# Optimization experiments

Hardware: AMD Instinct MI355X
Metric: run time of the kernel (lower is better)

The kernel has to match this reference:

```python
import jax, jax.numpy as jnp
import numpy as np
from itertools import product

N_VOX = 100000
GRID = 128
KS = 3
K = KS ** 3
INC_MAX, OUTC_MAX = 64, 96
RUNTIME_INC, RUNTIME_OUTC = 48, 64


def _build_rulebook(rng):
    flat = rng.choice(GRID ** 3, size=N_VOX, replace=False).astype(np.int64)
    coords = np.stack(np.unravel_index(flat, (GRID, GRID, GRID)), axis=1)  # [N,3]
    # Dense lookup table: flat coord -> voxel index (or -1).
    table = np.full(GRID ** 3, -1, dtype=np.int32)
    table[flat] = np.arange(N_VOX, dtype=np.int32)
    offsets = np.array(list(product([-1, 0, 1], repeat=3)), dtype=np.int64)  # [27,3]
    idx = np.empty((K, N_VOX), dtype=np.int32)
    for k, off in enumerate(offsets):
        nb = coords + off  # stride=1, dilation=1
        valid = np.all((nb >= 0) & (nb < GRID), axis=1)
        nb_flat = (nb[:, 0] * GRID + nb[:, 1]) * GRID + nb[:, 2]
        nb_flat = np.where(valid, nb_flat, 0)
        idx[k] = np.where(valid, table[nb_flat], -1)
    return idx


def setup_inputs() -> dict:
    key = jax.random.key(0)
    kf, kw = jax.random.split(key)
    features = jax.random.normal(kf, (N_VOX, RUNTIME_INC), dtype=jnp.float32)
    # Full kernel param [K, inc_max, outc_max]; runtime-sliced inside reference.
    std = 1.0 / np.sqrt(INC_MAX * K)
    kernel = jax.random.uniform(kw, (K, INC_MAX, OUTC_MAX), dtype=jnp.float32,
                                minval=-std, maxval=std)
    idx = jnp.asarray(_build_rulebook(np.random.default_rng(0)))  # [K, N]
    return {"features": features, "kernel": kernel, "idx": idx,
            "runtime_inc": RUNTIME_INC, "runtime_outc": RUNTIME_OUTC}


def reference(features, kernel, idx, runtime_inc, runtime_outc):
    # Dynamic channel slicing (static Python ints -> jit friendly).
    w = kernel[:, :runtime_inc, :runtime_outc]          # [K, Ci, Co]
    mask = idx >= 0                                      # [K, N]
    safe = jnp.where(mask, idx, 0)
    # Gather -> per-offset GEMM -> accumulate (scatter is identity: out idx == n).
    gathered = features[safe] * mask[..., None].astype(features.dtype)  # [K, N, Ci]
    out = jnp.einsum('knc,kco->no', gathered, w)         # [N, Co]
    return out
```

## Files before the change

### kernel.cpp

```cpp
#include <hip/hip_runtime.h>
#include <hip/hip_bf16.h>


#define NVOX       100000
#define INC        48
#define INC_MAX    64
#define OUTC       64
#define OUTC_MAX   96
#define KOFF       27
#define FEAT_ROW   64
#define FEATB_ELEMS ((NVOX + 1) * FEAT_ROW)
#define WTB_ELEMS  (KOFF * 4096)
#define WS_NEED    ((size_t)(FEATB_ELEMS + WTB_ELEMS) * 2)
#define FEAT_THREADS ((NVOX + 1) * 8)
#define FEAT_PREP_BLKS ((FEAT_THREADS + 255) / 256)
#define WTB_PREP_BLKS  432
#define MAIN_BLOCKS 782

typedef __attribute__((ext_vector_type(8))) short  short8;
typedef __attribute__((ext_vector_type(4))) float  floatx4;

__device__ __forceinline__ short f2bf(float f) {
    union { __hip_bfloat16 h; short s; } u;
    u.h = __float2bfloat16(f);
    return u.s;
}

__global__ void __launch_bounds__(256)
prep_cvt(const float* __restrict__ feat, const float* __restrict__ wk,
         short* __restrict__ featb, short* __restrict__ wtb)
{
    int b = blockIdx.x;
    if (b < FEAT_PREP_BLKS) {
        int t = b * 256 + threadIdx.x;
        if (t < FEAT_THREADS) {
            int g = t >> 3, c8 = (t & 7) * 8;
            short8 p = (short8){0, 0, 0, 0, 0, 0, 0, 0};
            if (g < NVOX && c8 < INC) {
                const floatx4* src = (const floatx4*)(feat + g * INC + c8);
                floatx4 f0 = src[0], f1 = src[1];
                #pragma unroll
                for (int j = 0; j < 4; ++j) { p[j] = f2bf(f0[j]); p[4 + j] = f2bf(f1[j]); }
            }
            *(short8*)(featb + g * FEAT_ROW + c8) = p;
        }
    } else {
        int t = (b - FEAT_PREP_BLKS) * 256 + threadIdx.x;
        int k = t >> 12, r = t & 4095;
        int frag = r >> 9, lane = (r >> 3) & 63, j = t & 7;
        int ks = frag >> 2, nt = frag & 3, quad = lane >> 4, l16 = lane & 15;
        int o = nt * 16 + l16, c = ks * 32 + quad * 8 + j;
        wtb[t] = (c < INC) ? f2bf(wk[k * (INC_MAX * OUTC_MAX) + c * OUTC_MAX + o])
                           : (short)0;
    }
}

__global__ void __launch_bounds__(256, 3)
spconv_main(const short* __restrict__ featb, const short* __restrict__ wtb,
            const int* __restrict__ idx, float* __restrict__ out)
{
    __shared__ short Bs[2][2][4096];

    const int tid  = threadIdx.x;
    const int lane = tid & 63;
    const int wave = tid >> 6;
    const int quad = lane >> 4;
    const int l16  = lane & 15;

    int bid = blockIdx.x;
    int sb  = (bid < 776) ? ((bid & 7) * 97 + (bid >> 3)) : bid;

    const int m0 = (sb * 4 + wave) * 32;
    const int r0 = m0 + l16;
    const int r1 = m0 + 16 + l16;
    const bool v0 = r0 < NVOX, v1 = r1 < NVOX;
    const int rr0 = v0 ? r0 : 0;
    const int rr1 = v1 ? r1 : 0;

    floatx4 acc[2][4];
    #pragma unroll
    for (int i = 0; i < 2; ++i)
        #pragma unroll
        for (int j = 0; j < 4; ++j)
            acc[i][j] = (floatx4){0.f, 0.f, 0.f, 0.f};

    short8 A[4][2][2];
    short8 bst[4][2];
    int    row0[4], row1[4];

    auto ldrow = [&](int k) {
        int t0 = idx[k * NVOX + rr0];
        int t1 = idx[k * NVOX + rr1];
        row0[k & 3] = (t0 < 0) ? NVOX : t0;
        row1[k & 3] = (t1 < 0) ? NVOX : t1;
    };
    auto aload = [&](int k) {
        const short8* p0 = (const short8*)(featb + row0[k & 3] * FEAT_ROW);
        const short8* p1 = (const short8*)(featb + row1[k & 3] * FEAT_ROW);
        A[k & 3][0][0] = p0[quad];  A[k & 3][0][1] = p0[quad + 4];
        A[k & 3][1][0] = p1[quad];  A[k & 3][1][1] = p1[quad + 4];
    };
    auto bload = [&](int k) {
        bst[k & 3][0] = *(const short8*)(wtb + k * 4096 + tid * 8);
        bst[k & 3][1] = *(const short8*)(wtb + k * 4096 + tid * 8 + 2048);
    };
    auto compute = [&](int k, int pb, int sub) {
        #pragma unroll
        for (int ks = 0; ks < 2; ++ks) {
            short8 b[4];
            #pragma unroll
            for (int nt = 0; nt < 4; ++nt)
                b[nt] = *(const short8*)&Bs[pb][sub][(ks * 4 + nt) * 512 + lane * 8];
            #pragma unroll
            for (int mt = 0; mt < 2; ++mt)
                #pragma unroll
                for (int nt = 0; nt < 4; ++nt)
                    acc[mt][nt] = __builtin_amdgcn_mfma_f32_16x16x32_bf16(
                        A[k & 3][mt][ks], b[nt], acc[mt][nt], 0, 0, 0);
        }
    };

    ldrow(0); ldrow(1); ldrow(2); ldrow(3);
    aload(0); aload(1);
    bload(0); bload(1);

    #pragma unroll
    for (int j = 0; j < 14; ++j) {
        const int kk = 2 * j;
        const int pb = j & 1;

        *(short8*)&Bs[pb][0][tid * 8]        = bst[kk & 3][0];
        *(short8*)&Bs[pb][0][tid * 8 + 2048] = bst[kk & 3][1];
        if (kk + 1 < KOFF) {
            *(short8*)&Bs[pb][1][tid * 8]        = bst[(kk + 1) & 3][0];
            *(short8*)&Bs[pb][1][tid * 8 + 2048] = bst[(kk + 1) & 3][1];
        }
        __syncthreads();

        if (kk + 2 < KOFF) { aload(kk + 2); bload(kk + 2); }
        if (kk + 3 < KOFF) { aload(kk + 3); bload(kk + 3); }
        if (kk + 4 < KOFF) ldrow(kk + 4);
        if (kk + 5 < KOFF) ldrow(kk + 5);

        compute(kk, pb, 0);
        if (kk + 1 < KOFF) compute(kk + 1, pb, 1);
    }

    #pragma unroll
    for (int mt = 0; mt < 2; ++mt) {
        int gbase = m0 + mt * 16 + quad * 4;
        #pragma unroll
        for (int r = 0; r < 4; ++r) {
            if (gbase + r < NVOX) {
                #pragma unroll
                for (int nt = 0; nt < 4; ++nt)
                    out[(gbase + r) * OUTC + nt * 16 + l16] = acc[mt][nt][r];
            }
        }
    }
}

__global__ void __launch_bounds__(256)
spconv_fallback(const float* __restrict__ feat, const float* __restrict__ wk,
                const int* __restrict__ idx, float* __restrict__ out)
{
    int t = blockIdx.x * 256 + threadIdx.x;
    if (t >= NVOX * OUTC) return;
    int n = t >> 6, o = t & 63;
    float s = 0.f;
    for (int k = 0; k < KOFF; ++k) {
        int g = idx[k * NVOX + n];
        if (g >= 0) {
            const float* fr = feat + g * INC;
            const float* wr = wk + k * (INC_MAX * OUTC_MAX) + o;
            #pragma unroll 8
            for (int c = 0; c < INC; ++c) s += fr[c] * wr[c * OUTC_MAX];
        }
    }
    out[t] = s;
}

extern "C" void kernel_launch(void* const* d_in, const int* in_sizes, int n_in,
                              void* d_out, int out_size, void* d_ws, size_t ws_size,
                              hipStream_t stream) {
    const float* feat = (const float*)d_in[0];
    const float* wk   = (const float*)d_in[1];
    const int*   idx  = (const int*)d_in[2];
    float* out = (float*)d_out;

    if (ws_size >= WS_NEED) {
        short* featb = (short*)d_ws;
        short* wtb   = featb + FEATB_ELEMS;
        prep_cvt<<<FEAT_PREP_BLKS + WTB_PREP_BLKS, 256, 0, stream>>>(feat, wk, featb, wtb);
        spconv_main<<<MAIN_BLOCKS, 256, 0, stream>>>(featb, wtb, idx, out);
    } else {
        spconv_fallback<<<(NVOX * OUTC + 255) / 256, 256, 0, stream>>>(feat, wk, idx, out);
    }
}
```

Before: 115.0 us.

## Switch to 32x32x16 MFMA with unpadded 48-channel weights and 4-slot LDS ring

Replaces the 16x16x32 bf16 MFMA tiling with 32x32x16 MFMA, so each wave covers its 32 rows with two accumulator tiles. The K dimension now uses the real 48 input channels as three k-steps instead of padding to 64, which cuts MFMA work, A-gather loads and weight bytes by a quarter. The LDS weight buffer becomes a 4-slot ring with a smaller per-offset footprint, and feature gathers are issued after compute to hold fewer A registers. The risks are the new fragment layout mapping and the different output store pattern with 32-lane column writes.

```diff
diff --git a/kernel.cpp b/kernel.cpp
--- a/kernel.cpp
+++ b/kernel.cpp
@@ -10,15 +10,17 @@
 #define KOFF       27
 #define FEAT_ROW   64
 #define FEATB_ELEMS ((NVOX + 1) * FEAT_ROW)
-#define WTB_ELEMS  (KOFF * 4096)
+#define WTB_K      3072
+#define WTB_ELEMS  (KOFF * WTB_K)
 #define WS_NEED    ((size_t)(FEATB_ELEMS + WTB_ELEMS) * 2)
 #define FEAT_THREADS ((NVOX + 1) * 8)
 #define FEAT_PREP_BLKS ((FEAT_THREADS + 255) / 256)
-#define WTB_PREP_BLKS  432
+#define WTB_PREP_BLKS  (WTB_ELEMS / 256)
 #define MAIN_BLOCKS 782
 
-typedef __attribute__((ext_vector_type(8))) short  short8;
-typedef __attribute__((ext_vector_type(4))) float  floatx4;
+typedef __attribute__((ext_vector_type(8)))  short short8;
+typedef __attribute__((ext_vector_type(4)))  float floatx4;
+typedef __attribute__((ext_vector_type(16))) float floatx16;
 
 __device__ __forceinline__ short f2bf(float f) {
     union { __hip_bfloat16 h; short s; } u;
@@ -46,12 +48,13 @@
         }
     } else {
         int t = (b - FEAT_PREP_BLKS) * 256 + threadIdx.x;
-        int k = t >> 12, r = t & 4095;
-        int frag = r >> 9, lane = (r >> 3) & 63, j = t & 7;
-        int ks = frag >> 2, nt = frag & 3, quad = lane >> 4, l16 = lane & 15;
-        int o = nt * 16 + l16, c = ks * 32 + quad * 8 + j;
-        wtb[t] = (c < INC) ? f2bf(wk[k * (INC_MAX * OUTC_MAX) + c * OUTC_MAX + o])
-                           : (short)0;
+        int k = t / WTB_K, r = t % WTB_K;
+        int chunk = r >> 3, j = r & 7;
+        int f = chunk >> 6, lane = chunk & 63;
+        int ks = f >> 1, nt = f & 1;
+        int c = ks * 16 + (lane >> 5) * 8 + j;
+        int o = nt * 32 + (lane & 31);
+        wtb[t] = f2bf(wk[k * (INC_MAX * OUTC_MAX) + c * OUTC_MAX + o]);
     }
 }
 
@@ -59,102 +62,94 @@
 spconv_main(const short* __restrict__ featb, const short* __restrict__ wtb,
             const int* __restrict__ idx, float* __restrict__ out)
 {
-    __shared__ short Bs[2][2][4096];
+    __shared__ short Bs[4][WTB_K];
 
     const int tid  = threadIdx.x;
     const int lane = tid & 63;
     const int wave = tid >> 6;
-    const int quad = lane >> 4;
-    const int l16  = lane & 15;
+    const int l32  = lane & 31;
+    const int hi   = lane >> 5;
 
     int bid = blockIdx.x;
     int sb  = (bid < 776) ? ((bid & 7) * 97 + (bid >> 3)) : bid;
 
-    const int m0 = (sb * 4 + wave) * 32;
-    const int r0 = m0 + l16;
-    const int r1 = m0 + 16 + l16;
-    const bool v0 = r0 < NVOX, v1 = r1 < NVOX;
-    const int rr0 = v0 ? r0 : 0;
-    const int rr1 = v1 ? r1 : 0;
+    const int m0   = (sb * 4 + wave) * 32;
+    const bool act = (m0 < NVOX);
+    const int rr   = act ? (m0 + l32) : 0;
 
-    floatx4 acc[2][4];
+    floatx16 acc[2];
     #pragma unroll
-    for (int i = 0; i < 2; ++i)
+    for (int nt = 0; nt < 2; ++nt)
         #pragma unroll
-        for (int j = 0; j < 4; ++j)
-            acc[i][j] = (floatx4){0.f, 0.f, 0.f, 0.f};
+        for (int r = 0; r < 16; ++r) acc[nt][r] = 0.f;
 
-    short8 A[4][2][2];
-    short8 bst[4][2];
-    int    row0[4], row1[4];
+    short8 A[2][3];
+    short8 bst[2][2];
+    int    rowg[4];
 
     auto ldrow = [&](int k) {
-        int t0 = idx[k * NVOX + rr0];
-        int t1 = idx[k * NVOX + rr1];
-        row0[k & 3] = (t0 < 0) ? NVOX : t0;
-        row1[k & 3] = (t1 < 0) ? NVOX : t1;
+        int t0 = idx[k * NVOX + rr];
+        rowg[k & 3] = (t0 < 0) ? NVOX : t0;
     };
     auto aload = [&](int k) {
-        const short8* p0 = (const short8*)(featb + row0[k & 3] * FEAT_ROW);
-        const short8* p1 = (const short8*)(featb + row1[k & 3] * FEAT_ROW);
-        A[k & 3][0][0] = p0[quad];  A[k & 3][0][1] = p0[quad + 4];
-        A[k & 3][1][0] = p1[quad];  A[k & 3][1][1] = p1[quad + 4];
+        const short* p = featb + rowg[k & 3] * FEAT_ROW + hi * 8;
+        A[k & 1][0] = *(const short8*)(p);
+        A[k & 1][1] = *(const short8*)(p + 16);
+        A[k & 1][2] = *(const short8*)(p + 32);
     };
     auto bload = [&](int k) {
-        bst[k & 3][0] = *(const short8*)(wtb + k * 4096 + tid * 8);
-        bst[k & 3][1] = *(const short8*)(wtb + k * 4096 + tid * 8 + 2048);
+        bst[k & 1][0] = *(const short8*)(wtb + k * WTB_K + tid * 8);
+        if (tid < 128)
+            bst[k & 1][1] = *(const short8*)(wtb + k * WTB_K + 2048 + tid * 8);
     };
-    auto compute = [&](int k, int pb, int sub) {
+    auto compute = [&](int k) {
         #pragma unroll
-        for (int ks = 0; ks < 2; ++ks) {
-            short8 b[4];
-            #pragma unroll
-            for (int nt = 0; nt < 4; ++nt)
-                b[nt] = *(const short8*)&Bs[pb][sub][(ks * 4 + nt) * 512 + lane * 8];
-            #pragma unroll
-            for (int mt = 0; mt < 2; ++mt)
-                #pragma unroll
-                for (int nt = 0; nt < 4; ++nt)
-                    acc[mt][nt] = __builtin_amdgcn_mfma_f32_16x16x32_bf16(
-                        A[k & 3][mt][ks], b[nt], acc[mt][nt], 0, 0, 0);
+        for (int ks = 0; ks < 3; ++ks) {
+            short8 b0 = *(const short8*)&Bs[k & 3][(ks * 128 + lane) * 8];
+            short8 b1 = *(const short8*)&Bs[k & 3][(ks * 128 + 64 + lane) * 8];
+            acc[0] = __builtin_amdgcn_mfma_f32_32x32x16_bf16(
+                A[k & 1][ks], b0, acc[0], 0, 0, 0);
+            acc[1] = __builtin_amdgcn_mfma_f32_32x32x16_bf16(
+                A[k & 1][ks], b1, acc[1], 0, 0, 0);
         }
     };
 
     ldrow(0); ldrow(1); ldrow(2); ldrow(3);
+    bload(0); bload(1);
     aload(0); aload(1);
-    bload(0); bload(1);
 
     #pragma unroll
     for (int j = 0; j < 14; ++j) {
         const int kk = 2 * j;
-        const int pb = j & 1;
 
-        *(short8*)&Bs[pb][0][tid * 8]        = bst[kk & 3][0];
-        *(short8*)&Bs[pb][0][tid * 8 + 2048] = bst[kk & 3][1];
+        *(short8*)&Bs[kk & 3][tid * 8] = bst[0][0];
+        if (tid < 128) *(short8*)&Bs[kk & 3][2048 + tid * 8] = bst[0][1];
         if (kk + 1 < KOFF) {
-            *(short8*)&Bs[pb][1][tid * 8]        = bst[(kk + 1) & 3][0];
-            *(short8*)&Bs[pb][1][tid * 8 + 2048] = bst[(kk + 1) & 3][1];
+            *(short8*)&Bs[(kk + 1) & 3][tid * 8] = bst[1][0];
+            if (tid < 128) *(short8*)&Bs[(kk + 1) & 3][2048 + tid * 8] = bst[1][1];
         }
         __syncthreads();
 
-        if (kk + 2 < KOFF) { aload(kk + 2); bload(kk + 2); }
-        if (kk + 3 < KOFF) { aload(kk + 3); bload(kk + 3); }
+        if (kk + 2 < KOFF) bload(kk + 2);
+        if (kk + 3 < KOFF) bload(kk + 3);
         if (kk + 4 < KOFF) ldrow(kk + 4);
         if (kk + 5 < KOFF) ldrow(kk + 5);
 
-        compute(kk, pb, 0);
-        if (kk + 1 < KOFF) compute(kk + 1, pb, 1);
+        compute(kk);
+        if (kk + 2 < KOFF) aload(kk + 2);
+        if (kk + 1 < KOFF) {
+            compute(kk + 1);
+            if (kk + 3 < KOFF) aload(kk + 3);
+        }
     }
 
-    #pragma unroll
-    for (int mt = 0; mt < 2; ++mt) {
-        int gbase = m0 + mt * 16 + quad * 4;
+    if (act) {
         #pragma unroll
-        for (int r = 0; r < 4; ++r) {
-            if (gbase + r < NVOX) {
-                #pragma unroll
-                for (int nt = 0; nt < 4; ++nt)
-                    out[(gbase + r) * OUTC + nt * 16 + l16] = acc[mt][nt][r];
+        for (int nt = 0; nt < 2; ++nt) {
+            #pragma unroll
+            for (int r = 0; r < 16; ++r) {
+                int row = (r & 3) + 8 * (r >> 2) + 4 * hi;
+                out[(m0 + row) * OUTC + nt * 32 + l32] = acc[nt][r];
             }
         }
     }
```

Result: faster. 108.4 us (-5.8%).
